# Performance work log

Hardware: AMD Instinct MI355X
Metric: run time of the kernel (lower is better)

## Reference

```python
import jax, jax.numpy as jnp
import numpy as np

EMBED = 768
HEADS = 12


def setup_inputs() -> dict:
    key = jax.random.key(0)
    k1, k2, k3, k4, k5 = jax.random.split(key, 5)
    B, N, E = 8, 1024, EMBED
    x = jax.random.normal(k1, (B, N, E), dtype=jnp.float32)
    # torch Linear stored as [in, out] here (math-equivalent: y = x @ W + b)
    w_qkv = jax.random.normal(k2, (E, 3 * E), dtype=jnp.float32) * (E ** -0.5)
    b_qkv = jax.random.normal(k3, (3 * E,), dtype=jnp.float32) * 0.02
    w_proj = jax.random.normal(k4, (E, E), dtype=jnp.float32) * (E ** -0.5)
    b_proj = jax.random.normal(k5, (E,), dtype=jnp.float32) * 0.02
    return {"x": x, "w_qkv": w_qkv, "b_qkv": b_qkv, "w_proj": w_proj, "b_proj": b_proj}


def reference(x, w_qkv, b_qkv, w_proj, b_proj):
    B, N, E = x.shape
    H = HEADS
    D = E // H
    qkv = x @ w_qkv + b_qkv                       # [B, N, 3E]
    # rearrange 'b n (h d qkv) -> qkv b h n d': qkv index is innermost in last dim
    qkv = qkv.reshape(B, N, H, D, 3)
    qkv = jnp.transpose(qkv, (4, 0, 2, 1, 3))      # [3, B, H, N, D]
    q, k, v = qkv[0], qkv[1], qkv[2]
    energy = jnp.einsum('bhqd,bhkd->bhqk', q, k)   # [B, H, N, N]
    scaling = float(E) ** 0.5
    # NOTE: original scales AFTER softmax (unusual but faithful)
    att = jax.nn.softmax(energy, axis=-1) / scaling
    # dropout_prob = 0.0 -> identity
    out = jnp.einsum('bhqk,bhkd->bhqd', att, v)    # [B, H, N, D]
    out = jnp.transpose(out, (0, 2, 1, 3)).reshape(B, N, E)
    return out @ w_proj + b_proj
```

## Files before the change

### kernel.cpp

```cpp
#include <hip/hip_runtime.h>
#include <hip/hip_bf16.h>
#include <stdint.h>

#define NSEQ 1024
#define EMB 768
#define HEADS 12
#define HD 64
#define BATCH 8
#define BHN (BATCH*HEADS)

typedef __attribute__((ext_vector_type(8))) short bf16x8;
typedef __attribute__((ext_vector_type(4))) short bf16x4;
typedef __attribute__((ext_vector_type(4))) float f32x4;

typedef const void __attribute__((address_space(1))) cglobal_void;
typedef void __attribute__((address_space(3))) lds_void_t;

#define LOG2E 1.4426950408889634f

__device__ __forceinline__ void load_lds16(const void* g, void* l) {
    __builtin_amdgcn_global_load_lds((cglobal_void*)g, (lds_void_t*)l, 16, 0, 0);
}

__device__ __forceinline__ unsigned short f2bf(float f) {
    __hip_bfloat16 h = __float2bfloat16(f);
    return *reinterpret_cast<unsigned short*>(&h);
}

__device__ __forceinline__ float exp2_hw(float x) {
#if __has_builtin(__builtin_amdgcn_exp2f)
    return __builtin_amdgcn_exp2f(x);
#else
    return exp2f(x);
#endif
}

__global__ void conv_x_kernel(const float* __restrict__ x, unsigned short* __restrict__ xb) {
    int i = (blockIdx.x * 256 + threadIdx.x) * 4;
    float4 v = *reinterpret_cast<const float4*>(x + i);
    ushort4 o;
    o.x = f2bf(v.x); o.y = f2bf(v.y); o.z = f2bf(v.z); o.w = f2bf(v.w);
    *reinterpret_cast<ushort4*>(xb + i) = o;
}

template <int PERM>
__global__ void transpose_w_kernel(const float* __restrict__ w, unsigned short* __restrict__ wt,
                                   int K, int C) {
    __shared__ unsigned short tile[64][65];
    int c0 = blockIdx.x * 64;
    int k0 = blockIdx.y * 64;
    int t = threadIdx.x;
    int r = t >> 2, cc = (t & 3) * 16;
#pragma unroll
    for (int e = 0; e < 16; e += 4) {
        float4 v = *reinterpret_cast<const float4*>(w + (size_t)(k0 + r) * C + c0 + cc + e);
        float s0 = (PERM && ((c0 + cc + e + 0) % 3 == 0)) ? LOG2E : 1.0f;
        float s1 = (PERM && ((c0 + cc + e + 1) % 3 == 0)) ? LOG2E : 1.0f;
        float s2 = (PERM && ((c0 + cc + e + 2) % 3 == 0)) ? LOG2E : 1.0f;
        float s3 = (PERM && ((c0 + cc + e + 3) % 3 == 0)) ? LOG2E : 1.0f;
        tile[r][cc + e + 0] = f2bf(v.x * s0);
        tile[r][cc + e + 1] = f2bf(v.y * s1);
        tile[r][cc + e + 2] = f2bf(v.z * s2);
        tile[r][cc + e + 3] = f2bf(v.w * s3);
    }
    __syncthreads();
    int c = t >> 2, kk0 = (t & 3) * 16;
    int cg = c0 + c;
    int n;
    if (PERM) {
        int qkv = cg % 3, h = cg / 192, d = (cg % 192) / 3;
        n = qkv * EMB + h * HD + d;
    } else {
        n = cg;
    }
    uint4 lo, hi;
    lo.x = (unsigned)tile[kk0 + 0][c] | ((unsigned)tile[kk0 + 1][c] << 16);
    lo.y = (unsigned)tile[kk0 + 2][c] | ((unsigned)tile[kk0 + 3][c] << 16);
    lo.z = (unsigned)tile[kk0 + 4][c] | ((unsigned)tile[kk0 + 5][c] << 16);
    lo.w = (unsigned)tile[kk0 + 6][c] | ((unsigned)tile[kk0 + 7][c] << 16);
    hi.x = (unsigned)tile[kk0 + 8][c] | ((unsigned)tile[kk0 + 9][c] << 16);
    hi.y = (unsigned)tile[kk0 + 10][c] | ((unsigned)tile[kk0 + 11][c] << 16);
    hi.z = (unsigned)tile[kk0 + 12][c] | ((unsigned)tile[kk0 + 13][c] << 16);
    hi.w = (unsigned)tile[kk0 + 14][c] | ((unsigned)tile[kk0 + 15][c] << 16);
    *reinterpret_cast<uint4*>(wt + (size_t)n * K + k0 + kk0) = lo;
    *reinterpret_cast<uint4*>(wt + (size_t)n * K + k0 + kk0 + 8) = hi;
}

__global__ void perm_bias_kernel(const float* __restrict__ b, float* __restrict__ bp) {
    int c = blockIdx.x * 256 + threadIdx.x;
    int qkv = c % 3, h = c / 192, d = (c % 192) / 3;
    bp[qkv * EMB + h * HD + d] = (qkv == 0) ? b[c] * LOG2E : b[c];
}

template <int MODE>
__launch_bounds__(256, 4)
__global__ void gemm_bt_kernel(const unsigned short* __restrict__ A,
                               const unsigned short* __restrict__ Bt,
                               const float* __restrict__ bias,
                               float* __restrict__ out,
                               unsigned short* __restrict__ qout,
                               unsigned short* __restrict__ kout,
                               unsigned short* __restrict__ vout) {
    constexpr int TN = (MODE == 0) ? 18 : 6;
    constexpr int NWG = 64 * TN;
    constexpr int CHUNK = NWG / 8;
    constexpr int K = EMB;
    __shared__ unsigned short lds_a[128 * 64];
    __shared__ unsigned short lds_b[128 * 64];
    int bx0 = blockIdx.x;
    int bx = (bx0 % 8) * CHUNK + bx0 / 8;
    int tm = bx / TN, tn = bx % TN;
    bool vpath = (MODE == 0) && (tn >= 12);
    const unsigned short* Bt_eff = Bt + (vpath ? (size_t)1536 * K : (size_t)0);
    const float* bias_eff = bias + (vpath ? 1536 : 0);
    int n0 = (vpath ? tn - 12 : tn) * 128;
    int m0 = tm * 128;
    int t = threadIdx.x;
    int l = t & 63;
    int g = l >> 4, c16 = l & 15;
    int wr = (t >> 7) & 1, wc = (t >> 6) & 1;
    int wbase = (t & 192);

    const char* baseA_f = vpath ? (const char*)lds_b : (const char*)lds_a;
    const char* baseB_f = vpath ? (const char*)lds_a : (const char*)lds_b;
    int roA = (vpath ? wc : wr) * 64;
    int roB = (vpath ? wr : wc) * 64;

    f32x4 acc[4][4];
#pragma unroll
    for (int i = 0; i < 4; i++)
#pragma unroll
        for (int j = 0; j < 4; j++)
#pragma unroll
            for (int r = 0; r < 4; r++) acc[i][j][r] = 0.f;

    for (int kt = 0; kt < K; kt += 64) {
        __syncthreads();
#pragma unroll
        for (int i = 0; i < 4; i++) {
            int c = i * 256 + t;
            int row = c >> 3;
            int sc = ((c & 7) ^ (row & 7)) * 8;
            load_lds16(A + (size_t)(m0 + row) * K + kt + sc, lds_a + (size_t)(i * 256 + wbase) * 8);
            load_lds16(Bt_eff + (size_t)(n0 + row) * K + kt + sc, lds_b + (size_t)(i * 256 + wbase) * 8);
        }
        __syncthreads();
#pragma unroll
        for (int kk = 0; kk < 2; kk++) {
            int cb = kk * 64 + g * 16;
            bf16x8 fa[4], fb[4];
#pragma unroll
            for (int i = 0; i < 4; i++) {
                int row = roA + i * 16 + c16;
                fa[i] = *reinterpret_cast<const bf16x8*>(
                    baseA_f + row * 128 + (cb ^ ((row & 7) << 4)));
            }
#pragma unroll
            for (int j = 0; j < 4; j++) {
                int row = roB + j * 16 + c16;
                fb[j] = *reinterpret_cast<const bf16x8*>(
                    baseB_f + row * 128 + (cb ^ ((row & 7) << 4)));
            }
#pragma unroll
            for (int i = 0; i < 4; i++)
#pragma unroll
                for (int j = 0; j < 4; j++)
                    acc[i][j] = __builtin_amdgcn_mfma_f32_16x16x32_bf16(fa[i], fb[j], acc[i][j], 0, 0, 0);
        }
    }

    if (vpath) {
#pragma unroll
        for (int i = 0; i < 4; i++) {
#pragma unroll
            for (int r = 0; r < 4; r++) {
                int nv = wc * 64 + i * 16 + (g * 4) + r + n0;
                float bv = bias_eff[nv];
                int hh = nv >> 6, dd = nv & 63;
#pragma unroll
                for (int j = 0; j < 4; j++) {
                    int m_g = m0 + wr * 64 + j * 16 + c16;
                    int bb = m_g >> 10, nn = m_g & 1023;
                    int nnp = (nn & ~31) | ((nn & 12) << 1) | ((nn >> 2) & 4) | (nn & 3);
                    vout[((size_t)(bb * HEADS + hh) * HD + dd) * NSEQ + nnp] =
                        f2bf(acc[i][j][r] + bv);
                }
            }
        }
    } else {
#pragma unroll
        for (int i = 0; i < 4; i++) {
            int mbase = m0 + wr * 64 + i * 16 + (g * 4);
#pragma unroll
            for (int j = 0; j < 4; j++) {
                int n_g = n0 + wc * 64 + j * 16 + c16;
                float bv = bias_eff[n_g];
#pragma unroll
                for (int r = 0; r < 4; r++) {
                    int m_g = mbase + r;
                    float v = acc[i][j][r] + bv;
                    if (MODE == 0) {
                        int rem = n_g - ((n_g >= 768) ? 768 : 0);
                        int hh = rem >> 6, dd = rem & 63;
                        int bb = m_g >> 10, nn = m_g & 1023;
                        if (n_g < 768)
                            qout[(size_t)((bb * HEADS + hh) * NSEQ + nn) * HD + dd] = f2bf(v);
                        else
                            kout[(size_t)((bb * HEADS + hh) * NSEQ + nn) * HD + dd] = f2bf(v);
                    } else {
                        out[(size_t)m_g * EMB + n_g] = v;
                    }
                }
            }
        }
    }
}

__launch_bounds__(256, 3)
__global__ void attn_kernel(const unsigned short* __restrict__ Q,
                            const unsigned short* __restrict__ K,
                            const unsigned short* __restrict__ Vt,
                            unsigned short* __restrict__ Oout) {
    __shared__ unsigned short k_lds[2][64 * 64];
    __shared__ unsigned short vt_lds[2][64 * 64];
    int bx = blockIdx.x;
    int bh = bx % BHN;
    int q0 = (bx / BHN) << 7;
    int b = bh / HEADS, h = bh % HEADS;
    int t = threadIdx.x, w = t >> 6, l = t & 63;
    int g = l >> 4, c16 = l & 15;
    const unsigned short* Qh = Q + (size_t)bh * NSEQ * HD;
    const unsigned short* Kh = K + (size_t)bh * NSEQ * HD;
    const unsigned short* Vth = Vt + (size_t)bh * NSEQ * HD;

    int qrA = q0 + w * 32 + c16;
    int qrB = qrA + 16;
    bf16x8 qfA[2], qfB[2];
    qfA[0] = *reinterpret_cast<const bf16x8*>(Qh + (size_t)qrA * HD + g * 8);
    qfA[1] = *reinterpret_cast<const bf16x8*>(Qh + (size_t)qrA * HD + 32 + g * 8);
    qfB[0] = *reinterpret_cast<const bf16x8*>(Qh + (size_t)qrB * HD + g * 8);
    qfB[1] = *reinterpret_cast<const bf16x8*>(Qh + (size_t)qrB * HD + 32 + g * 8);

    float lA = 0.f, lB = 0.f;
    f32x4 accA[4], accB[4];
#pragma unroll
    for (int jd = 0; jd < 4; jd++)
#pragma unroll
        for (int r = 0; r < 4; r++) { accA[jd][r] = 0.f; accB[jd][r] = 0.f; }

    auto stage = [&](int buf, int kv) {
#pragma unroll
        for (int i = 0; i < 2; i++) {
            int tt = i * 256 + t;
            int row = tt >> 3;
            int sc = ((tt & 7) ^ (row & 7)) * 8;
            load_lds16(Kh + (size_t)(kv + row) * HD + sc, k_lds[buf] + (size_t)(tt & ~63) * 8);
            load_lds16(Vth + (size_t)row * NSEQ + kv + sc, vt_lds[buf] + (size_t)(tt & ~63) * 8);
        }
    };

    stage(0, 0);
    __syncthreads();
    int cur = 0;
    for (int it = 0; it < 16; ++it) {
        if (it < 15) stage(cur ^ 1, (it + 1) << 6);

        const char* kbase = (const char*)k_lds[cur];
        const char* vbase = (const char*)vt_lds[cur];

        f32x4 stA[4], stB[4];
#pragma unroll
        for (int jk = 0; jk < 4; jk++)
#pragma unroll
            for (int r = 0; r < 4; r++) { stA[jk][r] = 0.f; stB[jk][r] = 0.f; }
        __builtin_amdgcn_s_setprio(1);
#pragma unroll
        for (int kk = 0; kk < 2; kk++) {
            int cb = kk * 64 + g * 16;
#pragma unroll
            for (int jk = 0; jk < 4; jk++) {
                int row = jk * 16 + c16;
                bf16x8 kf = *reinterpret_cast<const bf16x8*>(
                    kbase + row * 128 + (cb ^ ((row & 7) << 4)));
                stA[jk] = __builtin_amdgcn_mfma_f32_16x16x32_bf16(kf, qfA[kk], stA[jk], 0, 0, 0);
                stB[jk] = __builtin_amdgcn_mfma_f32_16x16x32_bf16(kf, qfB[kk], stB[jk], 0, 0, 0);
            }
        }
        __builtin_amdgcn_s_setprio(0);

#pragma unroll
        for (int jk = 0; jk < 4; jk++)
#pragma unroll
            for (int r = 0; r < 4; r++) {
                stA[jk][r] = exp2_hw(stA[jk][r]);
                stB[jk][r] = exp2_hw(stB[jk][r]);
            }

        bf16x8 pfA[2], pfB[2];
#pragma unroll
        for (int r = 0; r < 4; r++) {
            pfA[0][r] = (short)f2bf(stA[0][r]); pfA[0][4 + r] = (short)f2bf(stA[1][r]);
            pfA[1][r] = (short)f2bf(stA[2][r]); pfA[1][4 + r] = (short)f2bf(stA[3][r]);
            pfB[0][r] = (short)f2bf(stB[0][r]); pfB[0][4 + r] = (short)f2bf(stB[1][r]);
            pfB[1][r] = (short)f2bf(stB[2][r]); pfB[1][4 + r] = (short)f2bf(stB[3][r]);
        }

        __builtin_amdgcn_s_setprio(1);
#pragma unroll
        for (int ks = 0; ks < 2; ks++) {
            int cb = ks * 64 + g * 16;
#pragma unroll
            for (int jd = 0; jd < 4; jd++) {
                int row = jd * 16 + c16;
                bf16x8 vf = *reinterpret_cast<const bf16x8*>(
                    vbase + row * 128 + (cb ^ ((row & 7) << 4)));
                accA[jd] = __builtin_amdgcn_mfma_f32_16x16x32_bf16(vf, pfA[ks], accA[jd], 0, 0, 0);
                accB[jd] = __builtin_amdgcn_mfma_f32_16x16x32_bf16(vf, pfB[ks], accB[jd], 0, 0, 0);
            }
        }
        __builtin_amdgcn_s_setprio(0);

        float psA = (((stA[0][0] + stA[0][1]) + (stA[0][2] + stA[0][3])) +
                     ((stA[1][0] + stA[1][1]) + (stA[1][2] + stA[1][3]))) +
                    (((stA[2][0] + stA[2][1]) + (stA[2][2] + stA[2][3])) +
                     ((stA[3][0] + stA[3][1]) + (stA[3][2] + stA[3][3])));
        float psB = (((stB[0][0] + stB[0][1]) + (stB[0][2] + stB[0][3])) +
                     ((stB[1][0] + stB[1][1]) + (stB[1][2] + stB[1][3]))) +
                    (((stB[2][0] + stB[2][1]) + (stB[2][2] + stB[2][3])) +
                     ((stB[3][0] + stB[3][1]) + (stB[3][2] + stB[3][3])));
        psA += __shfl_xor(psA, 16);
        psA += __shfl_xor(psA, 32);
        psB += __shfl_xor(psB, 16);
        psB += __shfl_xor(psB, 32);
        lA += psA;
        lB += psB;

        __syncthreads();
        cur ^= 1;
    }

    const float scale = 27.712812921102035f;
    float invA = 1.0f / (lA * scale);
    float invB = 1.0f / (lB * scale);
    size_t qbaseA = ((size_t)(b * NSEQ + qrA) * HEADS + h) * HD;
    size_t qbaseB = ((size_t)(b * NSEQ + qrB) * HEADS + h) * HD;
#pragma unroll
    for (int jd = 0; jd < 4; jd++)
#pragma unroll
        for (int r = 0; r < 4; r++) {
            int d = jd * 16 + g * 4 + r;
            Oout[qbaseA + d] = f2bf(accA[jd][r] * invA);
            Oout[qbaseB + d] = f2bf(accB[jd][r] * invB);
        }
}

extern "C" void kernel_launch(void* const* d_in, const int* in_sizes, int n_in,
                              void* d_out, int out_size, void* d_ws, size_t ws_size,
                              hipStream_t stream) {
    const float* x = (const float*)d_in[0];
    const float* w_qkv = (const float*)d_in[1];
    const float* b_qkv = (const float*)d_in[2];
    const float* w_proj = (const float*)d_in[3];
    const float* b_proj = (const float*)d_in[4];

    char* ws = (char*)d_ws;
    unsigned short* xb      = (unsigned short*)(ws + 0);
    unsigned short* wt_qkv  = (unsigned short*)(ws + 12582912);
    unsigned short* wt_proj = (unsigned short*)(ws + 16121856);
    float*          biasp   = (float*)(ws + 17301504);
    unsigned short* qb      = (unsigned short*)(ws + 17310720);
    unsigned short* kb      = (unsigned short*)(ws + 29893632);
    unsigned short* vtb     = (unsigned short*)(ws + 42476544);
    unsigned short* ao      = (unsigned short*)(ws + 55059456);

    conv_x_kernel<<<6144, 256, 0, stream>>>(x, xb);
    transpose_w_kernel<1><<<dim3(36, 12), 256, 0, stream>>>(w_qkv, wt_qkv, EMB, 3 * EMB);
    transpose_w_kernel<0><<<dim3(12, 12), 256, 0, stream>>>(w_proj, wt_proj, EMB, EMB);
    perm_bias_kernel<<<9, 256, 0, stream>>>(b_qkv, biasp);

    gemm_bt_kernel<0><<<64 * 18, 256, 0, stream>>>(xb, wt_qkv, biasp, nullptr, qb, kb, vtb);
    attn_kernel<<<BHN * 8, 256, 0, stream>>>(qb, kb, vtb, ao);
    gemm_bt_kernel<1><<<64 * 6, 256, 0, stream>>>(ao, wt_proj, b_proj, (float*)d_out,
                                                  nullptr, nullptr, nullptr);
}
```

Baseline: 105.7 us.

## Add dedicated 64x128 projection GEMM and cheapen attention softmax conversions

Replaces the templated projection GEMM with a dedicated kernel using 64x128 tiles and 768 workgroups, up from 384, to fill more compute units on the small output GEMM. In the attention kernel, packs P into bf16 with the packed v_cvt_pk_bf16_f32 instruction instead of per-element conversions. It also defers the cross-lane row-sum shuffles out of the KV loop to the end. Smaller projection tiles mean less data reuse per workgroup and more total traffic for A and B.

```diff
diff --git a/kernel.cpp b/kernel.cpp
--- a/kernel.cpp
+++ b/kernel.cpp
@@ -25,6 +25,12 @@
 __device__ __forceinline__ unsigned short f2bf(float f) {
     __hip_bfloat16 h = __float2bfloat16(f);
     return *reinterpret_cast<unsigned short*>(&h);
+}
+
+__device__ __forceinline__ unsigned int cvt_pk_bf16(float lo, float hi) {
+    unsigned int r;
+    asm("v_cvt_pk_bf16_f32 %0, %1, %2" : "=v"(r) : "v"(lo), "v"(hi));
+    return r;
 }
 
 __device__ __forceinline__ float exp2_hw(float x) {
@@ -92,16 +98,14 @@
     bp[qkv * EMB + h * HD + d] = (qkv == 0) ? b[c] * LOG2E : b[c];
 }
 
-template <int MODE>
 __launch_bounds__(256, 4)
-__global__ void gemm_bt_kernel(const unsigned short* __restrict__ A,
-                               const unsigned short* __restrict__ Bt,
-                               const float* __restrict__ bias,
-                               float* __restrict__ out,
-                               unsigned short* __restrict__ qout,
-                               unsigned short* __restrict__ kout,
-                               unsigned short* __restrict__ vout) {
-    constexpr int TN = (MODE == 0) ? 18 : 6;
+__global__ void gemm_qkv_kernel(const unsigned short* __restrict__ A,
+                                const unsigned short* __restrict__ Bt,
+                                const float* __restrict__ bias,
+                                unsigned short* __restrict__ qout,
+                                unsigned short* __restrict__ kout,
+                                unsigned short* __restrict__ vout) {
+    constexpr int TN = 18;
     constexpr int NWG = 64 * TN;
     constexpr int CHUNK = NWG / 8;
     constexpr int K = EMB;
@@ -110,7 +114,7 @@
     int bx0 = blockIdx.x;
     int bx = (bx0 % 8) * CHUNK + bx0 / 8;
     int tm = bx / TN, tn = bx % TN;
-    bool vpath = (MODE == 0) && (tn >= 12);
+    bool vpath = (tn >= 12);
     const unsigned short* Bt_eff = Bt + (vpath ? (size_t)1536 * K : (size_t)0);
     const float* bias_eff = bias + (vpath ? 1536 : 0);
     int n0 = (vpath ? tn - 12 : tn) * 128;
@@ -199,19 +203,99 @@
                 for (int r = 0; r < 4; r++) {
                     int m_g = mbase + r;
                     float v = acc[i][j][r] + bv;
-                    if (MODE == 0) {
-                        int rem = n_g - ((n_g >= 768) ? 768 : 0);
-                        int hh = rem >> 6, dd = rem & 63;
-                        int bb = m_g >> 10, nn = m_g & 1023;
-                        if (n_g < 768)
-                            qout[(size_t)((bb * HEADS + hh) * NSEQ + nn) * HD + dd] = f2bf(v);
-                        else
-                            kout[(size_t)((bb * HEADS + hh) * NSEQ + nn) * HD + dd] = f2bf(v);
-                    } else {
-                        out[(size_t)m_g * EMB + n_g] = v;
-                    }
+                    int rem = n_g - ((n_g >= 768) ? 768 : 0);
+                    int hh = rem >> 6, dd = rem & 63;
+                    int bb = m_g >> 10, nn = m_g & 1023;
+                    if (n_g < 768)
+                        qout[(size_t)((bb * HEADS + hh) * NSEQ + nn) * HD + dd] = f2bf(v);
+                    else
+                        kout[(size_t)((bb * HEADS + hh) * NSEQ + nn) * HD + dd] = f2bf(v);
                 }
             }
+        }
+    }
+}
+
+__launch_bounds__(256, 4)
+__global__ void proj_kernel(const unsigned short* __restrict__ A,
+                            const unsigned short* __restrict__ Bt,
+                            const float* __restrict__ bias,
+                            float* __restrict__ out) {
+    constexpr int TN = 6;
+    constexpr int NWG = 128 * TN;
+    constexpr int CHUNK = NWG / 8;
+    constexpr int K = EMB;
+    __shared__ unsigned short lds_a[64 * 64];
+    __shared__ unsigned short lds_b[128 * 64];
+    int bx0 = blockIdx.x;
+    int bx = (bx0 % 8) * CHUNK + bx0 / 8;
+    int tm = bx / TN, tn = bx % TN;
+    int m0 = tm * 64, n0 = tn * 128;
+    int t = threadIdx.x;
+    int l = t & 63;
+    int g = l >> 4, c16 = l & 15;
+    int w = t >> 6;
+    int wbase = (t & 192);
+
+    f32x4 acc[4][2];
+#pragma unroll
+    for (int i = 0; i < 4; i++)
+#pragma unroll
+        for (int j = 0; j < 2; j++)
+#pragma unroll
+            for (int r = 0; r < 4; r++) acc[i][j][r] = 0.f;
+
+    for (int kt = 0; kt < K; kt += 64) {
+        __syncthreads();
+#pragma unroll
+        for (int i = 0; i < 2; i++) {
+            int c = i * 256 + t;
+            int row = c >> 3;
+            int sc = ((c & 7) ^ (row & 7)) * 8;
+            load_lds16(A + (size_t)(m0 + row) * K + kt + sc, lds_a + (size_t)(i * 256 + wbase) * 8);
+        }
+#pragma unroll
+        for (int i = 0; i < 4; i++) {
+            int c = i * 256 + t;
+            int row = c >> 3;
+            int sc = ((c & 7) ^ (row & 7)) * 8;
+            load_lds16(Bt + (size_t)(n0 + row) * K + kt + sc, lds_b + (size_t)(i * 256 + wbase) * 8);
+        }
+        __syncthreads();
+#pragma unroll
+        for (int kk = 0; kk < 2; kk++) {
+            int cb = kk * 64 + g * 16;
+            bf16x8 fa[4], fb[2];
+#pragma unroll
+            for (int i = 0; i < 4; i++) {
+                int row = i * 16 + c16;
+                fa[i] = *reinterpret_cast<const bf16x8*>(
+                    (const char*)lds_a + row * 128 + (cb ^ ((row & 7) << 4)));
+            }
+#pragma unroll
+            for (int j = 0; j < 2; j++) {
+                int row = w * 32 + j * 16 + c16;
+                fb[j] = *reinterpret_cast<const bf16x8*>(
+                    (const char*)lds_b + row * 128 + (cb ^ ((row & 7) << 4)));
+            }
+#pragma unroll
+            for (int i = 0; i < 4; i++)
+#pragma unroll
+                for (int j = 0; j < 2; j++)
+                    acc[i][j] = __builtin_amdgcn_mfma_f32_16x16x32_bf16(fa[i], fb[j], acc[i][j], 0, 0, 0);
+        }
+    }
+
+#pragma unroll
+    for (int i = 0; i < 4; i++) {
+        int mbase = m0 + i * 16 + g * 4;
+#pragma unroll
+        for (int j = 0; j < 2; j++) {
+            int n_g = n0 + w * 32 + j * 16 + c16;
+            float bv = bias[n_g];
+#pragma unroll
+            for (int r = 0; r < 4; r++)
+                out[(size_t)(mbase + r) * EMB + n_g] = acc[i][j][r] + bv;
         }
     }
 }
@@ -296,14 +380,21 @@
                 stB[jk][r] = exp2_hw(stB[jk][r]);
             }
 
-        bf16x8 pfA[2], pfB[2];
-#pragma unroll
-        for (int r = 0; r < 4; r++) {
-            pfA[0][r] = (short)f2bf(stA[0][r]); pfA[0][4 + r] = (short)f2bf(stA[1][r]);
-            pfA[1][r] = (short)f2bf(stA[2][r]); pfA[1][4 + r] = (short)f2bf(stA[3][r]);
-            pfB[0][r] = (short)f2bf(stB[0][r]); pfB[0][4 + r] = (short)f2bf(stB[1][r]);
-            pfB[1][r] = (short)f2bf(stB[2][r]); pfB[1][4 + r] = (short)f2bf(stB[3][r]);
-        }
+        union PU { unsigned int u[4]; bf16x8 v; };
+        PU puA0, puA1, puB0, puB1;
+#pragma unroll
+        for (int p = 0; p < 2; p++) {
+            puA0.u[p]     = cvt_pk_bf16(stA[0][2 * p], stA[0][2 * p + 1]);
+            puA0.u[2 + p] = cvt_pk_bf16(stA[1][2 * p], stA[1][2 * p + 1]);
+            puA1.u[p]     = cvt_pk_bf16(stA[2][2 * p], stA[2][2 * p + 1]);
+            puA1.u[2 + p] = cvt_pk_bf16(stA[3][2 * p], stA[3][2 * p + 1]);
+            puB0.u[p]     = cvt_pk_bf16(stB[0][2 * p], stB[0][2 * p + 1]);
+            puB0.u[2 + p] = cvt_pk_bf16(stB[1][2 * p], stB[1][2 * p + 1]);
+            puB1.u[p]     = cvt_pk_bf16(stB[2][2 * p], stB[2][2 * p + 1]);
+            puB1.u[2 + p] = cvt_pk_bf16(stB[3][2 * p], stB[3][2 * p + 1]);
+        }
+        bf16x8 pfA[2] = {puA0.v, puA1.v};
+        bf16x8 pfB[2] = {puB0.v, puB1.v};
 
         __builtin_amdgcn_s_setprio(1);
 #pragma unroll
@@ -320,25 +411,23 @@
         }
         __builtin_amdgcn_s_setprio(0);
 
-        float psA = (((stA[0][0] + stA[0][1]) + (stA[0][2] + stA[0][3])) +
-                     ((stA[1][0] + stA[1][1]) + (stA[1][2] + stA[1][3]))) +
-                    (((stA[2][0] + stA[2][1]) + (stA[2][2] + stA[2][3])) +
-                     ((stA[3][0] + stA[3][1]) + (stA[3][2] + stA[3][3])));
-        float psB = (((stB[0][0] + stB[0][1]) + (stB[0][2] + stB[0][3])) +
-                     ((stB[1][0] + stB[1][1]) + (stB[1][2] + stB[1][3]))) +
-                    (((stB[2][0] + stB[2][1]) + (stB[2][2] + stB[2][3])) +
-                     ((stB[3][0] + stB[3][1]) + (stB[3][2] + stB[3][3])));
-        psA += __shfl_xor(psA, 16);
-        psA += __shfl_xor(psA, 32);
-        psB += __shfl_xor(psB, 16);
-        psB += __shfl_xor(psB, 32);
-        lA += psA;
-        lB += psB;
+        lA += (((stA[0][0] + stA[0][1]) + (stA[0][2] + stA[0][3])) +
+               ((stA[1][0] + stA[1][1]) + (stA[1][2] + stA[1][3]))) +
+              (((stA[2][0] + stA[2][1]) + (stA[2][2] + stA[2][3])) +
+               ((stA[3][0] + stA[3][1]) + (stA[3][2] + stA[3][3])));
+        lB += (((stB[0][0] + stB[0][1]) + (stB[0][2] + stB[0][3])) +
+               ((stB[1][0] + stB[1][1]) + (stB[1][2] + stB[1][3]))) +
+              (((stB[2][0] + stB[2][1]) + (stB[2][2] + stB[2][3])) +
+               ((stB[3][0] + stB[3][1]) + (stB[3][2] + stB[3][3])));
 
         __syncthreads();
         cur ^= 1;
     }
 
+    lA += __shfl_xor(lA, 16);
+    lA += __shfl_xor(lA, 32);
+    lB += __shfl_xor(lB, 16);
+    lB += __shfl_xor(lB, 32);
     const float scale = 27.712812921102035f;
     float invA = 1.0f / (lA * scale);
     float invB = 1.0f / (lB * scale);
@@ -378,8 +467,7 @@
     transpose_w_kernel<0><<<dim3(12, 12), 256, 0, stream>>>(w_proj, wt_proj, EMB, EMB);
     perm_bias_kernel<<<9, 256, 0, stream>>>(b_qkv, biasp);
 
-    gemm_bt_kernel<0><<<64 * 18, 256, 0, stream>>>(xb, wt_qkv, biasp, nullptr, qb, kb, vtb);
+    gemm_qkv_kernel<<<64 * 18, 256, 0, stream>>>(xb, wt_qkv, biasp, qb, kb, vtb);
     attn_kernel<<<BHN * 8, 256, 0, stream>>>(qb, kb, vtb, ao);
-    gemm_bt_kernel<1><<<64 * 6, 256, 0, stream>>>(ao, wt_proj, b_proj, (float*)d_out,
-                                                  nullptr, nullptr, nullptr);
-}
+    proj_kernel<<<128 * 6, 256, 0, stream>>>(ao, wt_proj, b_proj, (float*)d_out);
+}
```

After: 103.7 us. About the same (-1.9%).
